# Kernel tuning notes

Measured on AMD Instinct MI355X. Metric: run time of the kernel, lower is better.

The kernel has to match this reference:

```python
import jax, jax.numpy as jnp
import numpy as np

H = 1024        # hidden_size
F = 4096        # intermediate_size
E = 8           # num_local_experts
TOP_K = 2       # num_experts_per_tok
B, S = 1, 2048


def setup_inputs() -> dict:
    key = jax.random.key(0)
    k0, k1, k2, k3 = jax.random.split(key, 4)
    hidden_states = jax.random.normal(k0, (B, S, H), dtype=jnp.float32)
    # torch nn.Linear weights: gate [E_out, in]; experts stacked on leading axis
    gate_w = jax.random.normal(k1, (E, H), dtype=jnp.float32) * 0.02
    gate_up_w = jax.random.normal(k2, (E, 2 * F, H), dtype=jnp.float32) * 0.02
    down_w = jax.random.normal(k3, (E, H, F), dtype=jnp.float32) * 0.02
    return {"hidden_states": hidden_states, "gate_w": gate_w,
            "gate_up_w": gate_up_w, "down_w": down_w}


def reference(hidden_states, gate_w, gate_up_w, down_w):
    b, s, h = hidden_states.shape
    x = hidden_states.reshape(-1, h)                      # [T, H]
    # router: softmax in float32, top-k, renormalize
    router_logits = x @ gate_w.T                          # [T, E]
    probs = jax.nn.softmax(router_logits.astype(jnp.float32), axis=-1)
    topw, sel = jax.lax.top_k(probs, TOP_K)               # [T, K]
    topw = topw / jnp.sum(topw, axis=-1, keepdims=True)
    topw = topw.astype(x.dtype)
    # combine weights [T, E]: zero for unselected experts -> same math as
    # the per-expert gather/scatter loop (full capacity, no dropped tokens)
    combine = jnp.sum(jax.nn.one_hot(sel, E, dtype=x.dtype) * topw[..., None], axis=1)
    # all experts on all tokens (dense-equivalent of masked dispatch)
    gu = jnp.einsum('th,efh->etf', x, gate_up_w)          # [E, T, 2F]
    gate, up = gu[..., :F], gu[..., F:]
    hact = up * jax.nn.gelu(gate, approximate=False)      # [E, T, F]
    expert_out = jnp.einsum('etf,ehf->eth', hact, down_w) # [E, T, H]
    out = jnp.einsum('eth,te->th', expert_out, combine)   # [T, H]
    return out.reshape(b, s, h)
```

## Files before the change

### kernel.cpp

```cpp
#include <hip/hip_runtime.h>

#define Hdim 1024
#define Fdim 4096
#define NE   8
#define NT   2048
#define MT_MAX 16

typedef __attribute__((ext_vector_type(8))) short short8;
typedef __attribute__((ext_vector_type(4))) short short4v;
typedef __attribute__((ext_vector_type(4))) float f32x4;

__device__ __forceinline__ unsigned short bf16r(float f) {
  union { float fv; unsigned u; } v; v.fv = f;
  unsigned u = v.u;
  return (unsigned short)((u + 0x7FFFu + ((u >> 16) & 1u)) >> 16);
}

__global__ void k_router(const float* __restrict__ x, const float* __restrict__ gw,
                         int* __restrict__ counts, int* __restrict__ sel,
                         float* __restrict__ selw) {
  int t = blockIdx.x;
  int l = threadIdx.x;
  const float* xp = x + (size_t)t * Hdim;
  float acc[NE];
#pragma unroll
  for (int e = 0; e < NE; e++) acc[e] = 0.f;
  for (int h = l; h < Hdim; h += 64) {
    float xv = xp[h];
#pragma unroll
    for (int e = 0; e < NE; e++) acc[e] += xv * gw[e * Hdim + h];
  }
#pragma unroll
  for (int e = 0; e < NE; e++) {
    float v = acc[e];
#pragma unroll
    for (int off = 32; off > 0; off >>= 1) v += __shfl_down(v, off, 64);
    acc[e] = v;
  }
  if (l == 0) {
    int b0 = 0; float v0 = acc[0];
    for (int e = 1; e < NE; e++) if (acc[e] > v0) { v0 = acc[e]; b0 = e; }
    int b1 = -1; float v1 = -1e30f;
    for (int e = 0; e < NE; e++) if (e != b0 && acc[e] > v1) { v1 = acc[e]; b1 = e; }
    float w0 = 1.f / (1.f + expf(v1 - v0));
    atomicAdd(&counts[b0], 1);
    atomicAdd(&counts[b1], 1);
    sel[2 * t]     = b0;
    sel[2 * t + 1] = b1;
    selw[2 * t]     = w0;
    selw[2 * t + 1] = 1.f - w0;
  }
}

__global__ void k_scan(const int* __restrict__ counts, int* __restrict__ offsets,
                       int* __restrict__ cursors) {
  if (threadIdx.x == 0) {
    int s = 0;
    for (int e = 0; e < NE; e++) { offsets[e] = s; s += counts[e]; cursors[e] = 0; }
  }
}

__global__ void k_scatter(const int* __restrict__ sel, const float* __restrict__ selw,
                          const int* __restrict__ offsets, int* __restrict__ cursors,
                          int* __restrict__ rowids, float* __restrict__ pairw) {
  int t = blockIdx.x * blockDim.x + threadIdx.x;
  if (t >= NT) return;
#pragma unroll
  for (int j = 0; j < 2; j++) {
    int e = sel[2 * t + j];
    float w = selw[2 * t + j];
    int p = atomicAdd(&cursors[e], 1);
    rowids[offsets[e] + p] = t;
    pairw[offsets[e] + p]  = w;
  }
}

__global__ __launch_bounds__(256, 2)
void k_gate_up(const float* __restrict__ x, const float* __restrict__ gup,
               const int* __restrict__ counts, const int* __restrict__ offsets,
               const int* __restrict__ rowids, unsigned short* __restrict__ hact) {
  int e  = blockIdx.y >> 4;
  int mt = blockIdx.y & 15;
  int n  = counts[e];
  if (mt * 128 >= n) return;
  int base = offsets[e];
  int row0 = mt * 128;
  int f0   = blockIdx.x * 64;

  __shared__ __align__(16) unsigned short As[128][32];
  __shared__ __align__(16) unsigned short Bs[128][32];
  __shared__ int rid[128];
  __shared__ float upbuf[2][64 * 65];

  int tid = threadIdx.x;
  if (tid < 128) {
    int r = row0 + tid;
    rid[tid] = (r < n) ? rowids[base + r] : rowids[base];
  }
  __syncthreads();

  int kc   = (tid & 7) * 4;
  int trow = tid >> 3;
  const float* ap[4];
  const float* bp[4];
#pragma unroll
  for (int p = 0; p < 4; p++) {
    int ar = p * 32 + trow;
    ap[p] = x + (size_t)rid[ar] * Hdim + kc;
    int f = (ar < 64) ? (f0 + ar) : (Fdim + f0 + (ar - 64));
    bp[p] = gup + ((size_t)e * 2 * Fdim + f) * Hdim + kc;
  }

  int wave = tid >> 6, lane = tid & 63;
  int wy = wave >> 1, wx = wave & 1;
  int lrow = lane & 15, lk = (lane >> 4) * 8;
  f32x4 acc[4][4] = {};

  for (int k0 = 0; k0 < Hdim; k0 += 32) {
    __syncthreads();
#pragma unroll
    for (int p = 0; p < 4; p++) {
      int ar = p * 32 + trow;
      float4 av = *(const float4*)(ap[p] + k0);
      short4v sa;
      sa.x = (short)bf16r(av.x); sa.y = (short)bf16r(av.y);
      sa.z = (short)bf16r(av.z); sa.w = (short)bf16r(av.w);
      *(short4v*)&As[ar][kc] = sa;
      float4 bv = *(const float4*)(bp[p] + k0);
      short4v sb;
      sb.x = (short)bf16r(bv.x); sb.y = (short)bf16r(bv.y);
      sb.z = (short)bf16r(bv.z); sb.w = (short)bf16r(bv.w);
      *(short4v*)&Bs[ar][kc] = sb;
    }
    __syncthreads();
    short8 a[4], b[4];
#pragma unroll
    for (int i = 0; i < 4; i++) a[i] = *(const short8*)&As[wy * 64 + i * 16 + lrow][lk];
#pragma unroll
    for (int j = 0; j < 4; j++) b[j] = *(const short8*)&Bs[wx * 64 + j * 16 + lrow][lk];
#pragma unroll
    for (int i = 0; i < 4; i++)
#pragma unroll
      for (int j = 0; j < 4; j++)
        acc[i][j] = __builtin_amdgcn_mfma_f32_16x16x32_bf16(a[i], b[j], acc[i][j], 0, 0, 0);
  }

  int quad = lane >> 4;
  if (wx == 1) {
#pragma unroll
    for (int i = 0; i < 4; i++)
#pragma unroll
      for (int j = 0; j < 4; j++)
#pragma unroll
        for (int r = 0; r < 4; r++)
          upbuf[wy][(i * 16 + quad * 4 + r) * 65 + j * 16 + lrow] = acc[i][j][r];
  }
  __syncthreads();
  if (wx == 0) {
#pragma unroll
    for (int i = 0; i < 4; i++) {
#pragma unroll
      for (int r = 0; r < 4; r++) {
        int rl = row0 + wy * 64 + i * 16 + quad * 4 + r;
        if (rl < n) {
          size_t rowoff = (size_t)(base + rl) * Fdim + f0;
#pragma unroll
          for (int j = 0; j < 4; j++) {
            float g = acc[i][j][r];
            float u = upbuf[wy][(i * 16 + quad * 4 + r) * 65 + j * 16 + lrow];
            float ge = 0.5f * g * (1.f + erff(g * 0.70710678118654752f));
            hact[rowoff + j * 16 + lrow] = bf16r(u * ge);
          }
        }
      }
    }
  }
}

__global__ __launch_bounds__(256, 2)
void k_down(const unsigned short* __restrict__ hact, const float* __restrict__ dw,
            const int* __restrict__ counts, const int* __restrict__ offsets,
            const int* __restrict__ rowids, const float* __restrict__ pairw,
            float* __restrict__ out) {
  int e  = blockIdx.y >> 4;
  int mt = blockIdx.y & 15;
  int n  = counts[e];
  if (mt * 128 >= n) return;
  int base = offsets[e];
  int row0 = mt * 128;
  int h0   = blockIdx.x * 128;

  __shared__ __align__(16) unsigned short As[128][32];
  __shared__ __align__(16) unsigned short Bs[128][32];

  int tid = threadIdx.x;
  int wave = tid >> 6, lane = tid & 63;
  int wy = wave >> 1, wx = wave & 1;
  int lrow = lane & 15, lk = (lane >> 4) * 8;

  const unsigned short* asrc[2];
#pragma unroll
  for (int p = 0; p < 2; p++) {
    int idx = p * 256 + tid;
    int row = idx >> 2, seg = idx & 3;
    int slot = base + row0 + row;
    if (slot > NT * 2 - 1) slot = NT * 2 - 1;
    asrc[p] = hact + (size_t)slot * Fdim + seg * 8;
  }
  int kc   = (tid & 7) * 4;
  int trow = tid >> 3;
  const float* bp[4];
#pragma unroll
  for (int p = 0; p < 4; p++) {
    int j = p * 32 + trow;
    bp[p] = dw + ((size_t)e * Hdim + h0 + j) * Fdim + kc;
  }

  f32x4 acc[4][4] = {};
  for (int k0 = 0; k0 < Fdim; k0 += 32) {
    __syncthreads();
#pragma unroll
    for (int p = 0; p < 2; p++) {
      int idx = p * 256 + tid;
      int row = idx >> 2, seg = idx & 3;
      *(int4*)&As[row][seg * 8] = *(const int4*)(asrc[p] + k0);
    }
#pragma unroll
    for (int p = 0; p < 4; p++) {
      int j = p * 32 + trow;
      float4 bv = *(const float4*)(bp[p] + k0);
      short4v sb;
      sb.x = (short)bf16r(bv.x); sb.y = (short)bf16r(bv.y);
      sb.z = (short)bf16r(bv.z); sb.w = (short)bf16r(bv.w);
      *(short4v*)&Bs[j][kc] = sb;
    }
    __syncthreads();
    short8 a[4], b[4];
#pragma unroll
    for (int i = 0; i < 4; i++) a[i] = *(const short8*)&As[wy * 64 + i * 16 + lrow][lk];
#pragma unroll
    for (int j = 0; j < 4; j++) b[j] = *(const short8*)&Bs[wx * 64 + j * 16 + lrow][lk];
#pragma unroll
    for (int i = 0; i < 4; i++)
#pragma unroll
      for (int j = 0; j < 4; j++)
        acc[i][j] = __builtin_amdgcn_mfma_f32_16x16x32_bf16(a[i], b[j], acc[i][j], 0, 0, 0);
  }

  int quad = lane >> 4;
#pragma unroll
  for (int i = 0; i < 4; i++) {
#pragma unroll
    for (int r = 0; r < 4; r++) {
      int rl = row0 + wy * 64 + i * 16 + quad * 4 + r;
      if (rl < n) {
        int slot = base + rl;
        int t    = rowids[slot];
        float wv = pairw[slot];
        float* op = out + (size_t)t * Hdim + h0 + wx * 64;
#pragma unroll
        for (int j = 0; j < 4; j++)
          atomicAdd(op + j * 16 + lrow, wv * acc[i][j][r]);
      }
    }
  }
}

extern "C" void kernel_launch(void* const* d_in, const int* in_sizes, int n_in,
                              void* d_out, int out_size, void* d_ws, size_t ws_size,
                              hipStream_t stream) {
  const float* x   = (const float*)d_in[0];
  const float* gw  = (const float*)d_in[1];
  const float* gup = (const float*)d_in[2];
  const float* dwn = (const float*)d_in[3];
  float* out = (float*)d_out;

  char* ws = (char*)d_ws;
  int*   counts  = (int*)(ws + 0);
  int*   cursors = (int*)(ws + 64);
  int*   offsets = (int*)(ws + 128);
  int*   sel     = (int*)(ws + 4096);
  float* selw    = (float*)(ws + 4096 + 16384);
  int*   rowids  = (int*)(ws + 4096 + 32768);
  float* pairw   = (float*)(ws + 4096 + 49152);
  unsigned short* hact = (unsigned short*)(ws + (1 << 20));

  hipMemsetAsync(ws, 0, 4096, stream);
  hipMemsetAsync(d_out, 0, (size_t)out_size * sizeof(float), stream);

  k_router<<<NT, 64, 0, stream>>>(x, gw, counts, sel, selw);
  k_scan<<<1, 64, 0, stream>>>(counts, offsets, cursors);
  k_scatter<<<(NT + 255) / 256, 256, 0, stream>>>(sel, selw, offsets, cursors, rowids, pairw);
  k_gate_up<<<dim3(Fdim / 64, NE * MT_MAX), 256, 0, stream>>>(x, gup, counts, offsets, rowids, hact);
  k_down<<<dim3(Hdim / 128, NE * MT_MAX), 256, 0, stream>>>(hact, dwn, counts, offsets, rowids, pairw, out);
}
```

Before: 857.3 us.

## Split-K down projection, fuse scan into scatter, drop gate/up LDS exchange

The down-projection GEMM is split along F into four z-slices, so grid occupancy rises; it relies on the existing atomicAdd output accumulation. Scan and scatter are merged into one single-block kernel that uses shared-memory cursors, which removes a launch. The router now processes four tokens per 256-thread block. In gate_up, each wave's B tiles are rearranged so that it holds matching gate and up columns in its own registers, removing the upbuf LDS round trip and a barrier. The cost is four times as many output atomics in k_down.

```diff
diff --git a/kernel.cpp b/kernel.cpp
--- a/kernel.cpp
+++ b/kernel.cpp
@@ -5,6 +5,7 @@
 #define NE   8
 #define NT   2048
 #define MT_MAX 16
+#define KSPLIT 4
 
 typedef __attribute__((ext_vector_type(8))) short short8;
 typedef __attribute__((ext_vector_type(4))) short short4v;
@@ -19,8 +20,9 @@
 __global__ void k_router(const float* __restrict__ x, const float* __restrict__ gw,
                          int* __restrict__ counts, int* __restrict__ sel,
                          float* __restrict__ selw) {
-  int t = blockIdx.x;
-  int l = threadIdx.x;
+  int wave = threadIdx.x >> 6;
+  int l    = threadIdx.x & 63;
+  int t    = blockIdx.x * 4 + wave;
   const float* xp = x + (size_t)t * Hdim;
   float acc[NE];
 #pragma unroll
@@ -52,26 +54,24 @@
   }
 }
 
-__global__ void k_scan(const int* __restrict__ counts, int* __restrict__ offsets,
-                       int* __restrict__ cursors) {
+__global__ void k_scatter(const int* __restrict__ counts, const int* __restrict__ sel,
+                          const float* __restrict__ selw, int* __restrict__ offsets,
+                          int* __restrict__ rowids, float* __restrict__ pairw) {
+  __shared__ int soff[NE];
+  __shared__ int scur[NE];
   if (threadIdx.x == 0) {
     int s = 0;
-    for (int e = 0; e < NE; e++) { offsets[e] = s; s += counts[e]; cursors[e] = 0; }
-  }
-}
-
-__global__ void k_scatter(const int* __restrict__ sel, const float* __restrict__ selw,
-                          const int* __restrict__ offsets, int* __restrict__ cursors,
-                          int* __restrict__ rowids, float* __restrict__ pairw) {
-  int t = blockIdx.x * blockDim.x + threadIdx.x;
-  if (t >= NT) return;
-#pragma unroll
-  for (int j = 0; j < 2; j++) {
-    int e = sel[2 * t + j];
-    float w = selw[2 * t + j];
-    int p = atomicAdd(&cursors[e], 1);
-    rowids[offsets[e] + p] = t;
-    pairw[offsets[e] + p]  = w;
+    for (int e = 0; e < NE; e++) { soff[e] = s; offsets[e] = s; s += counts[e]; scur[e] = 0; }
+  }
+  __syncthreads();
+  for (int t = threadIdx.x; t < NT; t += blockDim.x) {
+#pragma unroll
+    for (int j = 0; j < 2; j++) {
+      int e = sel[2 * t + j];
+      int p = atomicAdd(&scur[e], 1);
+      rowids[soff[e] + p] = t;
+      pairw[soff[e] + p]  = selw[2 * t + j];
+    }
   }
 }
 
@@ -90,7 +90,6 @@
   __shared__ __align__(16) unsigned short As[128][32];
   __shared__ __align__(16) unsigned short Bs[128][32];
   __shared__ int rid[128];
-  __shared__ float upbuf[2][64 * 65];
 
   int tid = threadIdx.x;
   if (tid < 128) {
@@ -136,8 +135,10 @@
     short8 a[4], b[4];
 #pragma unroll
     for (int i = 0; i < 4; i++) a[i] = *(const short8*)&As[wy * 64 + i * 16 + lrow][lk];
-#pragma unroll
-    for (int j = 0; j < 4; j++) b[j] = *(const short8*)&Bs[wx * 64 + j * 16 + lrow][lk];
+    b[0] = *(const short8*)&Bs[wx * 32 + lrow][lk];
+    b[1] = *(const short8*)&Bs[wx * 32 + 16 + lrow][lk];
+    b[2] = *(const short8*)&Bs[64 + wx * 32 + lrow][lk];
+    b[3] = *(const short8*)&Bs[64 + wx * 32 + 16 + lrow][lk];
 #pragma unroll
     for (int i = 0; i < 4; i++)
 #pragma unroll
@@ -146,31 +147,19 @@
   }
 
   int quad = lane >> 4;
-  if (wx == 1) {
-#pragma unroll
-    for (int i = 0; i < 4; i++)
-#pragma unroll
-      for (int j = 0; j < 4; j++)
-#pragma unroll
-        for (int r = 0; r < 4; r++)
-          upbuf[wy][(i * 16 + quad * 4 + r) * 65 + j * 16 + lrow] = acc[i][j][r];
-  }
-  __syncthreads();
-  if (wx == 0) {
-#pragma unroll
-    for (int i = 0; i < 4; i++) {
-#pragma unroll
-      for (int r = 0; r < 4; r++) {
-        int rl = row0 + wy * 64 + i * 16 + quad * 4 + r;
-        if (rl < n) {
-          size_t rowoff = (size_t)(base + rl) * Fdim + f0;
-#pragma unroll
-          for (int j = 0; j < 4; j++) {
-            float g = acc[i][j][r];
-            float u = upbuf[wy][(i * 16 + quad * 4 + r) * 65 + j * 16 + lrow];
-            float ge = 0.5f * g * (1.f + erff(g * 0.70710678118654752f));
-            hact[rowoff + j * 16 + lrow] = bf16r(u * ge);
-          }
+#pragma unroll
+  for (int i = 0; i < 4; i++) {
+#pragma unroll
+    for (int r = 0; r < 4; r++) {
+      int rl = row0 + wy * 64 + i * 16 + quad * 4 + r;
+      if (rl < n) {
+        size_t rowoff = (size_t)(base + rl) * Fdim + f0 + wx * 32;
+#pragma unroll
+        for (int j = 0; j < 2; j++) {
+          float g = acc[i][j][r];
+          float u = acc[i][j + 2][r];
+          float ge = 0.5f * g * (1.f + erff(g * 0.70710678118654752f));
+          hact[rowoff + j * 16 + lrow] = bf16r(u * ge);
         }
       }
     }
@@ -189,6 +178,8 @@
   int base = offsets[e];
   int row0 = mt * 128;
   int h0   = blockIdx.x * 128;
+  int kbeg = blockIdx.z * (Fdim / KSPLIT);
+  int kend = kbeg + Fdim / KSPLIT;
 
   __shared__ __align__(16) unsigned short As[128][32];
   __shared__ __align__(16) unsigned short Bs[128][32];
@@ -217,7 +208,7 @@
   }
 
   f32x4 acc[4][4] = {};
-  for (int k0 = 0; k0 < Fdim; k0 += 32) {
+  for (int k0 = kbeg; k0 < kend; k0 += 32) {
     __syncthreads();
 #pragma unroll
     for (int p = 0; p < 2; p++) {
@@ -277,7 +268,6 @@
 
   char* ws = (char*)d_ws;
   int*   counts  = (int*)(ws + 0);
-  int*   cursors = (int*)(ws + 64);
   int*   offsets = (int*)(ws + 128);
   int*   sel     = (int*)(ws + 4096);
   float* selw    = (float*)(ws + 4096 + 16384);
@@ -288,9 +278,8 @@
   hipMemsetAsync(ws, 0, 4096, stream);
   hipMemsetAsync(d_out, 0, (size_t)out_size * sizeof(float), stream);
 
-  k_router<<<NT, 64, 0, stream>>>(x, gw, counts, sel, selw);
-  k_scan<<<1, 64, 0, stream>>>(counts, offsets, cursors);
-  k_scatter<<<(NT + 255) / 256, 256, 0, stream>>>(sel, selw, offsets, cursors, rowids, pairw);
+  k_router<<<NT / 4, 256, 0, stream>>>(x, gw, counts, sel, selw);
+  k_scatter<<<1, 1024, 0, stream>>>(counts, sel, selw, offsets, rowids, pairw);
   k_gate_up<<<dim3(Fdim / 64, NE * MT_MAX), 256, 0, stream>>>(x, gup, counts, offsets, rowids, hact);
-  k_down<<<dim3(Hdim / 128, NE * MT_MAX), 256, 0, stream>>>(hact, dwn, counts, offsets, rowids, pairw, out);
-}
+  k_down<<<dim3(Hdim / 128, NE * MT_MAX, KSPLIT), 256, 0, stream>>>(hact, dwn, counts, offsets, rowids, pairw, out);
+}
```

Measured after the change: 865.0 us. About the same (+0.9%).
